# Performance work log

Hardware: AMD Instinct MI355X
Metric: run time of the kernel (lower is better)

The kernel has to match this reference:

```python
import jax, jax.numpy as jnp
import numpy as np

B, Tc, E, K, M, V = 8, 1024, 256, 8, 2048, 16
T1 = Tc * K          # penultimate layer length = 8192
TLAST = M * K        # last layer length = 16384


def setup_inputs() -> dict:
    key = jax.random.key(0)
    ks = jax.random.split(key, 12)
    x = jax.random.normal(ks[0], (B, Tc, E), jnp.float32)
    # penultimate values: exactly M 'mixed' tokens (value==2) per row, rest in {1,3}
    base = jnp.where(jnp.arange(T1) < M, 2, 1 + 2 * jax.random.randint(ks[1], (B, T1), 0, 2))
    perm = jnp.argsort(jax.random.uniform(ks[2], (B, T1)), axis=1)
    val1 = jnp.take_along_axis(base, perm, axis=1)
    vallast = 1 + 2 * jax.random.randint(ks[3], (B, TLAST), 0, 2)
    value = jnp.concatenate([val1, vallast], axis=1).astype(jnp.int64)
    depth = jnp.concatenate([jnp.full((B, T1), 5), jnp.full((B, TLAST), 6)], axis=1).astype(jnp.int64)
    pos = jax.random.randint(ks[4], (B, T1 + TLAST, 3), 0, 64).astype(jnp.int64)
    s = 0.02
    W1 = s * jax.random.normal(ks[5], (E, E, K), jnp.float32)  # ConvTranspose1d weight [in,out,k]
    b1 = s * jax.random.normal(ks[6], (E,), jnp.float32)
    W0 = s * jax.random.normal(ks[7], (E, E, K), jnp.float32)
    b0 = s * jax.random.normal(ks[8], (E,), jnp.float32)
    Wl = s * jax.random.normal(ks[9], (V + 1, E), jnp.float32)
    bl = s * jax.random.normal(ks[10], (V + 1,), jnp.float32)
    return {"x": x, "value": value, "depth": depth, "pos": pos, "num_mix": M,
            "W1": W1, "b1": b1, "W0": W0, "b0": b0, "Wl": Wl, "bl": bl}


def _deconv(x, W, b):
    # ConvTranspose1d with kernel=stride=K: each token expands to K tokens
    n, t, e = x.shape
    o = W.shape[1]
    y = jnp.einsum('nte,eoj->ntjo', x, W)  # [N,T,K,O]
    return y.reshape(n, t * W.shape[2], o) + b


def reference(x, value, depth, pos, num_mix, W1, b1, W0, b0, Wl, bl):
    n, tc, e = x.shape
    k = W1.shape[2]
    t1 = tc * k
    max_depth = jnp.max(depth)
    len_1 = jnp.sum(depth == max_depth - 1, axis=1)               # [N]
    tt = jnp.arange(t1)
    val_1 = jnp.where(tt[None, :] < len_1[:, None], value[:, :t1], 0)  # padded penultimate values
    mix_mask = val_1 == 2                                         # [N,T1]
    mix_1 = jnp.sum(mix_mask, axis=1)                             # [N]
    y_1 = _deconv(x, W1, b1)                                      # [N,T1,E]
    # stable pack: bring positions with value==2 to the front, keep order
    order = jnp.argsort(jnp.where(mix_mask, 0, 1), axis=1, stable=True)
    sel = order[:, :num_mix]                                      # [N,M]
    x_0 = jnp.take_along_axis(y_1, sel[:, :, None], axis=1)       # [N,M,E]
    valid = (jnp.arange(num_mix)[None, :] < mix_1[:, None]).astype(x_0.dtype)
    x_0 = x_0 * valid[:, :, None]                                 # zero-pad beyond per-row mix count
    y_0 = _deconv(x_0, W0, b0)                                    # [N,M*K,E]
    return y_0 @ Wl.T + bl                                        # [N,M*K,V+1]
```

## Files before the change

kernel.cpp:

```cpp
#include <hip/hip_runtime.h>

typedef __attribute__((ext_vector_type(8))) short bf16x8;
typedef __attribute__((ext_vector_type(4))) float f32x4;

#define BB 8
#define TC 1024
#define EE 256
#define KJ 8
#define MSEL 2048
#define V1 17
#define T1 8192
#define TTOT 24576
#define BI_TOT 16384
#define NCOLP 160
#define WSTRIDE 264

#define SCAL_OFF 0
#define GRP_OFF  1024
#define WFT_OFF  (GRP_OFF + 524288)
#define B2_OFF   (WFT_OFF + NCOLP*WSTRIDE*2)
#define BF0_OFF  (B2_OFF + 640)
#define WCT_OFF  (BF0_OFF + 128)

__device__ __forceinline__ unsigned short f2bf(float f) {
    union { float f; unsigned u; } x; x.f = f;
    unsigned r = x.u + 0x7fffu + ((x.u >> 16) & 1u);
    return (unsigned short)(r >> 16);
}
__device__ __forceinline__ float bf2f(unsigned short h) {
    union { unsigned u; float f; } x; x.u = ((unsigned)h) << 16;
    return x.f;
}

__global__ __launch_bounds__(256) void k_pre(const float* W0, const float* Wl, const int* depth,
                                             unsigned short* wfT, int* scal) {
    int bid = blockIdx.x, tid = threadIdx.x;
    __shared__ float w0s[EE * KJ];
    __shared__ float wls[V1 * 257];
    __shared__ int s_red[4];
    int em = bid;
    for (int idx = tid; idx < EE * KJ; idx += 256) w0s[idx] = W0[em * EE * KJ + idx];
    for (int idx = tid; idx < V1 * EE; idx += 256) {
        int v = idx >> 8, o = idx & 255;
        wls[v * 257 + o] = Wl[idx];
    }
    __syncthreads();
    if (tid < 136) {
        int j = tid / V1, v = tid - j * V1;
        float acc = 0.f;
        #pragma unroll 4
        for (int o = 0; o < EE; ++o) acc += w0s[o * KJ + j] * wls[v * 257 + o];
        wfT[(j * 20 + v) * WSTRIDE + em] = f2bf(acc);
    }
    if (bid < 8) {
        int b = bid;
        if (b == 0 && tid < 8) scal[33 + tid] = 0;
        const int4* dp = (const int4*)(depth + b * TTOT);
        int m = -2147483648;
        for (int i = tid; i < 6144; i += 256) {
            int4 d = dp[i];
            m = max(max(m, max(d.x, d.y)), max(d.z, d.w));
        }
        #pragma unroll
        for (int dd = 32; dd; dd >>= 1) m = max(m, __shfl_down(m, dd, 64));
        if ((tid & 63) == 0) s_red[tid >> 6] = m;
        __syncthreads();
        int bmax = max(max(s_red[0], s_red[1]), max(s_red[2], s_red[3]));
        if (tid == 0) scal[1 + b] = bmax;
        int c1 = 0, c2 = 0;
        for (int i = tid; i < 6144; i += 256) {
            int4 d = dp[i];
            c1 += (d.x == bmax) + (d.y == bmax) + (d.z == bmax) + (d.w == bmax);
            c2 += (d.x == bmax - 1) + (d.y == bmax - 1) + (d.z == bmax - 1) + (d.w == bmax - 1);
        }
        int cc = (c1 << 16) + c2;
        #pragma unroll
        for (int dd = 32; dd; dd >>= 1) cc += __shfl_down(cc, dd, 64);
        __syncthreads();
        if ((tid & 63) == 0) s_red[tid >> 6] = cc;
        __syncthreads();
        if (tid == 0) {
            int tot = s_red[0] + s_red[1] + s_red[2] + s_red[3];
            scal[9 + b] = tot >> 16;
            scal[17 + b] = tot & 0xffff;
        }
    }
}

__global__ __launch_bounds__(256) void k_mid(
        const int* value, const float* W1, const float* b1, const float* b0,
        const float* Wl, const float* bl,
        int* scal, int* groups, const unsigned short* wfT, float* bias2, float* bf0,
        unsigned short* wct) {
    int bid = blockIdx.x, tid = threadIdx.x;
    __shared__ __align__(16) unsigned short b1s[32 * WSTRIDE];
    __shared__ __align__(16) unsigned short af[NCOLP * WSTRIDE];
    __shared__ int s_wt[4], s_lcnt[8], s_lcnt2[8], s_lbase[8];
    if (bid < 64) {
        int g = bid >> 3;
        int e0 = (bid & 7) * 32;
        {
            int em_l = tid & 63;
            int eb = (tid >> 6) * 8;
            #pragma unroll
            for (int i = 0; i < 8; ++i) {
                int e = eb + i;
                #pragma unroll
                for (int c = 0; c < 4; ++c) {
                    int em = c * 64 + em_l;
                    b1s[e * WSTRIDE + em] = f2bf(W1[(e0 + e) * (EE * KJ) + em * KJ + g]);
                }
            }
        }
        for (int idx = tid; idx < 5120; idx += 256) {
            int row = idx >> 5, f = idx & 31;
            ((int4*)af)[row * 33 + f] = ((const int4*)wfT)[row * 33 + f];
        }
        __syncthreads();

        int w = tid >> 6, l = tid & 63;
        int ntile = w & 1, mhalf = w >> 1;
        int lr = l & 15, lq = l >> 4;
        f32x4 acc[5];
        #pragma unroll
        for (int t = 0; t < 5; ++t) acc[t] = (f32x4){0.f, 0.f, 0.f, 0.f};

        #pragma unroll
        for (int ch = 0; ch < 4; ++ch) {
            #pragma unroll
            for (int s = 0; s < 2; ++s) {
                bf16x8 bfr = *(const bf16x8*)&b1s[(ntile * 16 + lr) * WSTRIDE + ch * 64 + s * 32 + lq * 8];
                #pragma unroll
                for (int t = 0; t < 5; ++t) {
                    bf16x8 afr = *(const bf16x8*)&af[((mhalf * 5 + t) * 16 + lr) * WSTRIDE + ch * 64 + s * 32 + lq * 8];
                    acc[t] = __builtin_amdgcn_mfma_f32_16x16x32_bf16(afr, bfr, acc[t], 0, 0, 0);
                }
            }
        }
        #pragma unroll
        for (int t = 0; t < 5; ++t) {
            int m = (mhalf * 5 + t) * 16 + lq * 4;
            int n = e0 + ntile * 16 + lr;
            #pragma unroll
            for (int r = 0; r < 4; ++r)
                wct[(g * NCOLP + m + r) * WSTRIDE + n] = f2bf(acc[t][r]);
        }
        if (bid == 0) {
            for (int c = tid; c < NCOLP; c += 256) {
                int vv = c % 20;
                float s = 0.f;
                if (vv < V1) {
                    for (int e8 = 0; e8 < 32; ++e8) {
                        bf16x8 a8 = *(const bf16x8*)&af[c * WSTRIDE + e8 * 8];
                        #pragma unroll
                        for (int u = 0; u < 8; ++u)
                            s += b1[e8 * 8 + u] * bf2f((unsigned short)a8[u]);
                    }
                }
                bias2[c] = s;
            }
        } else if (bid == 1) {
            if (tid < V1) {
                float s = 0.f;
                #pragma unroll 4
                for (int e = 0; e < EE; ++e) s += b0[e] * Wl[tid * EE + e];
                bf0[tid] = s + bl[tid];
            }
        }
    } else {
        int b = bid - 64;
        int mb = scal[1 + b], cm = scal[9 + b], cm1 = scal[17 + b];
        int gmax = scal[1];
        #pragma unroll
        for (int q = 2; q <= 8; ++q) gmax = max(gmax, scal[q]);
        int len1 = (mb == gmax) ? cm1 : ((mb == gmax - 1) ? cm : 0);
        const int* vb = value + b * TTOT;
        int t0 = tid * 32;
        unsigned mask = 0;
        #pragma unroll
        for (int k = 0; k < 32; k += 4) {
            int4 v = *(const int4*)(vb + t0 + k);
            if (t0 + k + 0 < len1 && v.x == 2) mask |= 1u << (k + 0);
            if (t0 + k + 1 < len1 && v.y == 2) mask |= 1u << (k + 1);
            if (t0 + k + 2 < len1 && v.z == 2) mask |= 1u << (k + 2);
            if (t0 + k + 3 < len1 && v.w == 2) mask |= 1u << (k + 3);
        }
        int cnt = __popc(mask);
        int inc = cnt;
        #pragma unroll
        for (int d = 1; d < 64; d <<= 1) {
            int n = __shfl_up(inc, d, 64);
            if ((tid & 63) >= d) inc += n;
        }
        int lane = tid & 63, wid = tid >> 6;
        if (lane == 63) s_wt[wid] = inc;
        if (tid < 8) { s_lcnt[tid] = 0; s_lcnt2[tid] = 0; }
        __syncthreads();
        int woff = 0;
        for (int w = 0; w < wid; ++w) woff += s_wt[w];
        int off0 = woff + inc - cnt;
        int mix1 = s_wt[0] + s_wt[1] + s_wt[2] + s_wt[3];
        int mix1c = min(mix1, MSEL);
        {
            int off = off0;
            #pragma unroll
            for (int k = 0; k < 32; ++k) {
                if (mask & (1u << k)) {
                    if (off < MSEL) atomicAdd(&s_lcnt[(t0 + k) & 7], 1);
                    off++;
                }
            }
        }
        if (tid == 0 && mix1c < MSEL) atomicAdd(&s_lcnt[0], MSEL - mix1c);
        __syncthreads();
        if (tid < 8) s_lbase[tid] = atomicAdd(&scal[33 + tid], s_lcnt[tid]);
        __syncthreads();
        {
            int off = off0;
            #pragma unroll
            for (int k = 0; k < 32; ++k) {
                if (mask & (1u << k)) {
                    if (off < MSEL) {
                        int t = t0 + k;
                        int g = t & 7;
                        int ls = atomicAdd(&s_lcnt2[g], 1);
                        groups[g * BI_TOT + s_lbase[g] + ls] =
                            ((b * MSEL + off) << 11) | ((t >> 3) << 1) | 1;
                    }
                    off++;
                }
            }
        }
        for (int i = mix1c + tid; i < MSEL; i += 256) {
            int ls = atomicAdd(&s_lcnt2[0], 1);
            groups[s_lbase[0] + ls] = (b * MSEL + i) << 11;
        }
    }
}

__global__ __launch_bounds__(256) void k_main(const float* x, const unsigned short* wct,
        const int* scal, const int* groups, const float* bias2, const float* bf0, float* out) {
    int g = blockIdx.x >> 7;
    int tile0 = blockIdx.x & 127;
    int cntg = scal[33 + g];

    __shared__ __align__(16) unsigned short xs[32 * WSTRIDE];
    __shared__ __align__(16) unsigned short wts[NCOLP * 72];
    __shared__ int obase[32];
    __shared__ unsigned char vflag[32];
    int tid = threadIdx.x;
    const int4* wsrc = (const int4*)wct;
    int row8 = tid >> 3, q8 = tid & 7;
    int w = tid >> 6, l = tid & 63;
    int rw = w & 1, chalf = w >> 1;
    int lr = l & 15, lq = l >> 4;

    for (int tile = tile0; tile * 32 < cntg; tile += 128) {
        int nrows = min(32, cntg - tile * 32);
        int4 wreg[5];
        #pragma unroll
        for (int q = 0; q < 5; ++q)
            wreg[q] = wsrc[(g * NCOLP + row8 + q * 32) * 33 + q8];
        int pk = (row8 < nrows) ? groups[g * BI_TOT + tile * 32 + row8] : 0;
        int xo = ((pk >> 22) * TC + ((pk >> 1) & 1023)) * EE;
        float4 xr[8];
        #pragma unroll
        for (int i = 0; i < 8; ++i) xr[i] = *(const float4*)(x + xo + (q8 + 8 * i) * 4);

        __syncthreads();
        if (tid < 32) {
            int p2 = (tid < nrows) ? groups[g * BI_TOT + tile * 32 + tid] : 0;
            obase[tid] = (p2 >> 11) * 136;
            vflag[tid] = (tid < nrows) ? (unsigned char)(1 + (p2 & 1)) : (unsigned char)0;
        }
        #pragma unroll
        for (int i = 0; i < 8; ++i) {
            ushort4 pkv;
            pkv.x = f2bf(xr[i].x); pkv.y = f2bf(xr[i].y);
            pkv.z = f2bf(xr[i].z); pkv.w = f2bf(xr[i].w);
            *(ushort4*)&xs[row8 * WSTRIDE + (q8 + 8 * i) * 4] = pkv;
        }
        #pragma unroll
        for (int q = 0; q < 5; ++q)
            ((int4*)wts)[(row8 + q * 32) * 9 + q8] = wreg[q];
        #pragma unroll
        for (int q = 0; q < 5; ++q)
            wreg[q] = wsrc[(g * NCOLP + row8 + q * 32) * 33 + 8 + q8];
        __syncthreads();

        f32x4 acc[5];
        #pragma unroll
        for (int t = 0; t < 5; ++t) acc[t] = (f32x4){0.f, 0.f, 0.f, 0.f};

        for (int ch = 0; ch < 4; ++ch) {
            #pragma unroll
            for (int s = 0; s < 2; ++s) {
                bf16x8 afr = *(const bf16x8*)&xs[(rw * 16 + lr) * WSTRIDE + ch * 64 + s * 32 + lq * 8];
                #pragma unroll
                for (int t = 0; t < 5; ++t) {
                    bf16x8 bfr = *(const bf16x8*)&wts[((chalf * 5 + t) * 16 + lr) * 72 + s * 32 + lq * 8];
                    acc[t] = __builtin_amdgcn_mfma_f32_16x16x32_bf16(afr, bfr, acc[t], 0, 0, 0);
                }
            }
            if (ch < 3) {
                __syncthreads();
                #pragma unroll
                for (int q = 0; q < 5; ++q)
                    ((int4*)wts)[(row8 + q * 32) * 9 + q8] = wreg[q];
                if (ch < 2) {
                    #pragma unroll
                    for (int q = 0; q < 5; ++q)
                        wreg[q] = wsrc[(g * NCOLP + row8 + q * 32) * 33 + (ch + 2) * 8 + q8];
                }
                __syncthreads();
            }
        }
        #pragma unroll
        for (int t = 0; t < 5; ++t) {
            int col = (chalf * 5 + t) * 16 + lr;
            int j = col / 20, v = col % 20;
            if (v < V1) {
                float bb = bias2[col] + bf0[v];
                float b0v = bf0[v];
                #pragma unroll
                for (int r = 0; r < 4; ++r) {
                    int row = rw * 16 + lq * 4 + r;
                    int fl = vflag[row];
                    if (fl) out[obase[row] + j * V1 + v] = (fl == 2) ? (acc[t][r] + bb) : b0v;
                }
            }
        }
    }
}

extern "C" void kernel_launch(void* const* d_in, const int* in_sizes, int n_in,
                              void* d_out, int out_size, void* d_ws, size_t ws_size,
                              hipStream_t stream) {
    const float* x     = (const float*)d_in[0];
    const int*   value = (const int*)d_in[1];
    const int*   depth = (const int*)d_in[2];
    const float* W1    = (const float*)d_in[5];
    const float* b1    = (const float*)d_in[6];
    const float* W0    = (const float*)d_in[7];
    const float* b0    = (const float*)d_in[8];
    const float* Wl    = (const float*)d_in[9];
    const float* bl    = (const float*)d_in[10];
    float* out = (float*)d_out;
    char* ws = (char*)d_ws;

    int*            scal   = (int*)(ws + SCAL_OFF);
    int*            groups = (int*)(ws + GRP_OFF);
    unsigned short* wfT    = (unsigned short*)(ws + WFT_OFF);
    float*          bias2  = (float*)(ws + B2_OFF);
    float*          bf0    = (float*)(ws + BF0_OFF);
    unsigned short* wct    = (unsigned short*)(ws + WCT_OFF);

    k_pre <<<dim3(256),  dim3(256), 0, stream>>>(W0, Wl, depth, wfT, scal);
    k_mid <<<dim3(72),   dim3(256), 0, stream>>>(value, W1, b1, b0, Wl, bl,
                                                 scal, groups, wfT, bias2, bf0, wct);
    k_main<<<dim3(1024), dim3(256), 0, stream>>>(x, wct, scal, groups, bias2, bf0, out);
}
```

Before: 137.5 us.

## Pre-swizzle weights into MFMA fragment layout and read them directly from global

Stores the fused weight matrices (wfT and wct) in a packed layout that matches the MFMA operand fragment order, so each lane can load its bf16x8 operand straight from global memory. This removes the LDS staging, register double-buffering and per-chunk barriers in k_main and k_mid. It also moves the depth scan in k_pre to its own blocks and spreads the bias reductions (bias2, bf0) across extra k_mid blocks instead of doing them serially in one block. The cost is that weight reads now rely on L1/L2 hits rather than shared memory.

```diff
diff --git a/kernel.cpp b/kernel.cpp
--- a/kernel.cpp
+++ b/kernel.cpp
@@ -14,11 +14,16 @@
 #define BI_TOT 16384
 #define NCOLP 160
 #define WSTRIDE 264
+#define GSZ 40960
+
+__device__ __forceinline__ int pk_idx(int col, int e) {
+    return (((col >> 4) * 8 + (e >> 5)) << 9) + (((e >> 3) & 3) << 7) + ((col & 15) << 3) + (e & 7);
+}
 
 #define SCAL_OFF 0
 #define GRP_OFF  1024
 #define WFT_OFF  (GRP_OFF + 524288)
-#define B2_OFF   (WFT_OFF + NCOLP*WSTRIDE*2)
+#define B2_OFF   (WFT_OFF + GSZ*2)
 #define BF0_OFF  (B2_OFF + 640)
 #define WCT_OFF  (BF0_OFF + 128)
 
@@ -30,6 +35,18 @@
 __device__ __forceinline__ float bf2f(unsigned short h) {
     union { unsigned u; float f; } x; x.u = ((unsigned)h) << 16;
     return x.f;
+}
+
+__device__ __forceinline__ float blockReduceSum256(float v) {
+    __shared__ float sm[4];
+    #pragma unroll
+    for (int d = 32; d; d >>= 1) v += __shfl_down(v, d, 64);
+    int lane = threadIdx.x & 63, wid = threadIdx.x >> 6;
+    if (lane == 0) sm[wid] = v;
+    __syncthreads();
+    float r = sm[0] + sm[1] + sm[2] + sm[3];
+    __syncthreads();
+    return r;
 }
 
 __global__ __launch_bounds__(256) void k_pre(const float* W0, const float* Wl, const int* depth,
@@ -38,22 +55,23 @@
     __shared__ float w0s[EE * KJ];
     __shared__ float wls[V1 * 257];
     __shared__ int s_red[4];
-    int em = bid;
-    for (int idx = tid; idx < EE * KJ; idx += 256) w0s[idx] = W0[em * EE * KJ + idx];
-    for (int idx = tid; idx < V1 * EE; idx += 256) {
-        int v = idx >> 8, o = idx & 255;
-        wls[v * 257 + o] = Wl[idx];
-    }
-    __syncthreads();
-    if (tid < 136) {
-        int j = tid / V1, v = tid - j * V1;
-        float acc = 0.f;
-        #pragma unroll 4
-        for (int o = 0; o < EE; ++o) acc += w0s[o * KJ + j] * wls[v * 257 + o];
-        wfT[(j * 20 + v) * WSTRIDE + em] = f2bf(acc);
-    }
-    if (bid < 8) {
-        int b = bid;
+    if (bid < 256) {
+        int em = bid;
+        for (int idx = tid; idx < EE * KJ; idx += 256) w0s[idx] = W0[em * EE * KJ + idx];
+        for (int idx = tid; idx < V1 * EE; idx += 256) {
+            int v = idx >> 8, o = idx & 255;
+            wls[v * 257 + o] = Wl[idx];
+        }
+        __syncthreads();
+        if (tid < 136) {
+            int j = tid / V1, v = tid - j * V1;
+            float acc = 0.f;
+            #pragma unroll 4
+            for (int o = 0; o < EE; ++o) acc += w0s[o * KJ + j] * wls[v * 257 + o];
+            wfT[pk_idx(j * 20 + v, em)] = f2bf(acc);
+        }
+    } else {
+        int b = bid - 256;
         if (b == 0 && tid < 8) scal[33 + tid] = 0;
         const int4* dp = (const int4*)(depth + b * TTOT);
         int m = -2147483648;
@@ -94,7 +112,6 @@
         unsigned short* wct) {
     int bid = blockIdx.x, tid = threadIdx.x;
     __shared__ __align__(16) unsigned short b1s[32 * WSTRIDE];
-    __shared__ __align__(16) unsigned short af[NCOLP * WSTRIDE];
     __shared__ int s_wt[4], s_lcnt[8], s_lcnt2[8], s_lbase[8];
     if (bid < 64) {
         int g = bid >> 3;
@@ -112,10 +129,6 @@
                 }
             }
         }
-        for (int idx = tid; idx < 5120; idx += 256) {
-            int row = idx >> 5, f = idx & 31;
-            ((int4*)af)[row * 33 + f] = ((const int4*)wfT)[row * 33 + f];
-        }
         __syncthreads();
 
         int w = tid >> 6, l = tid & 63;
@@ -132,42 +145,22 @@
                 bf16x8 bfr = *(const bf16x8*)&b1s[(ntile * 16 + lr) * WSTRIDE + ch * 64 + s * 32 + lq * 8];
                 #pragma unroll
                 for (int t = 0; t < 5; ++t) {
-                    bf16x8 afr = *(const bf16x8*)&af[((mhalf * 5 + t) * 16 + lr) * WSTRIDE + ch * 64 + s * 32 + lq * 8];
+                    bf16x8 afr = *(const bf16x8*)&wfT[(((mhalf * 5 + t) * 8 + ch * 2 + s) << 9) + l * 8];
                     acc[t] = __builtin_amdgcn_mfma_f32_16x16x32_bf16(afr, bfr, acc[t], 0, 0, 0);
                 }
             }
         }
         #pragma unroll
         for (int t = 0; t < 5; ++t) {
-            int m = (mhalf * 5 + t) * 16 + lq * 4;
-            int n = e0 + ntile * 16 + lr;
-            #pragma unroll
-            for (int r = 0; r < 4; ++r)
-                wct[(g * NCOLP + m + r) * WSTRIDE + n] = f2bf(acc[t][r]);
-        }
-        if (bid == 0) {
-            for (int c = tid; c < NCOLP; c += 256) {
-                int vv = c % 20;
-                float s = 0.f;
-                if (vv < V1) {
-                    for (int e8 = 0; e8 < 32; ++e8) {
-                        bf16x8 a8 = *(const bf16x8*)&af[c * WSTRIDE + e8 * 8];
-                        #pragma unroll
-                        for (int u = 0; u < 8; ++u)
-                            s += b1[e8 * 8 + u] * bf2f((unsigned short)a8[u]);
-                    }
-                }
-                bias2[c] = s;
-            }
-        } else if (bid == 1) {
-            if (tid < V1) {
-                float s = 0.f;
-                #pragma unroll 4
-                for (int e = 0; e < EE; ++e) s += b0[e] * Wl[tid * EE + e];
-                bf0[tid] = s + bl[tid];
-            }
-        }
-    } else {
+            int ct = mhalf * 5 + t;
+            int e = e0 + ntile * 16 + lr;
+            #pragma unroll
+            for (int r = 0; r < 4; ++r) {
+                int col = ct * 16 + lq * 4 + r;
+                wct[g * GSZ + pk_idx(col, e)] = f2bf(acc[t][r]);
+            }
+        }
+    } else if (bid < 72) {
         int b = bid - 64;
         int mb = scal[1 + b], cm = scal[9 + b], cm1 = scal[17 + b];
         int gmax = scal[1];
@@ -235,6 +228,19 @@
             int ls = atomicAdd(&s_lcnt2[0], 1);
             groups[s_lbase[0] + ls] = (b * MSEL + i) << 11;
         }
+    } else if (bid < 89) {
+        int v = bid - 72;
+        float s = blockReduceSum256(b0[tid] * Wl[v * EE + tid]);
+        if (tid == 0) bf0[v] = s + bl[v];
+    } else {
+        #pragma unroll
+        for (int r = 0; r < 2; ++r) {
+            int c17 = (bid - 89) * 2 + r;
+            int j = c17 / V1, v = c17 - j * V1;
+            int colP = j * 20 + v;
+            float s = blockReduceSum256(b1[tid] * bf2f(wfT[pk_idx(colP, tid)]));
+            if (tid == 0) bias2[colP] = s;
+        }
     }
 }
 
@@ -245,34 +251,30 @@
     int cntg = scal[33 + g];
 
     __shared__ __align__(16) unsigned short xs[32 * WSTRIDE];
-    __shared__ __align__(16) unsigned short wts[NCOLP * 72];
     __shared__ int obase[32];
     __shared__ unsigned char vflag[32];
     int tid = threadIdx.x;
-    const int4* wsrc = (const int4*)wct;
     int row8 = tid >> 3, q8 = tid & 7;
     int w = tid >> 6, l = tid & 63;
     int rw = w & 1, chalf = w >> 1;
     int lr = l & 15, lq = l >> 4;
+    const unsigned short* wg = wct + g * GSZ;
 
     for (int tile = tile0; tile * 32 < cntg; tile += 128) {
         int nrows = min(32, cntg - tile * 32);
-        int4 wreg[5];
-        #pragma unroll
-        for (int q = 0; q < 5; ++q)
-            wreg[q] = wsrc[(g * NCOLP + row8 + q * 32) * 33 + q8];
+        __syncthreads();
         int pk = (row8 < nrows) ? groups[g * BI_TOT + tile * 32 + row8] : 0;
-        int xo = ((pk >> 22) * TC + ((pk >> 1) & 1023)) * EE;
-        float4 xr[8];
-        #pragma unroll
-        for (int i = 0; i < 8; ++i) xr[i] = *(const float4*)(x + xo + (q8 + 8 * i) * 4);
-
-        __syncthreads();
         if (tid < 32) {
             int p2 = (tid < nrows) ? groups[g * BI_TOT + tile * 32 + tid] : 0;
             obase[tid] = (p2 >> 11) * 136;
             vflag[tid] = (tid < nrows) ? (unsigned char)(1 + (p2 & 1)) : (unsigned char)0;
         }
+        int bi = pk >> 11;
+        int xo = ((bi >> 11) * TC + ((pk >> 1) & 1023)) * EE;
+        const float* xp = x + xo;
+        float4 xr[8];
+        #pragma unroll
+        for (int i = 0; i < 8; ++i) xr[i] = *(const float4*)(xp + (q8 + 8 * i) * 4);
         #pragma unroll
         for (int i = 0; i < 8; ++i) {
             ushort4 pkv;
@@ -280,39 +282,21 @@
             pkv.z = f2bf(xr[i].z); pkv.w = f2bf(xr[i].w);
             *(ushort4*)&xs[row8 * WSTRIDE + (q8 + 8 * i) * 4] = pkv;
         }
-        #pragma unroll
-        for (int q = 0; q < 5; ++q)
-            ((int4*)wts)[(row8 + q * 32) * 9 + q8] = wreg[q];
-        #pragma unroll
-        for (int q = 0; q < 5; ++q)
-            wreg[q] = wsrc[(g * NCOLP + row8 + q * 32) * 33 + 8 + q8];
         __syncthreads();
 
         f32x4 acc[5];
         #pragma unroll
         for (int t = 0; t < 5; ++t) acc[t] = (f32x4){0.f, 0.f, 0.f, 0.f};
-
+        #pragma unroll
         for (int ch = 0; ch < 4; ++ch) {
             #pragma unroll
             for (int s = 0; s < 2; ++s) {
                 bf16x8 afr = *(const bf16x8*)&xs[(rw * 16 + lr) * WSTRIDE + ch * 64 + s * 32 + lq * 8];
                 #pragma unroll
                 for (int t = 0; t < 5; ++t) {
-                    bf16x8 bfr = *(const bf16x8*)&wts[((chalf * 5 + t) * 16 + lr) * 72 + s * 32 + lq * 8];
+                    bf16x8 bfr = *(const bf16x8*)&wg[(((chalf * 5 + t) * 8 + ch * 2 + s) << 9) + l * 8];
                     acc[t] = __builtin_amdgcn_mfma_f32_16x16x32_bf16(afr, bfr, acc[t], 0, 0, 0);
                 }
-            }
-            if (ch < 3) {
-                __syncthreads();
-                #pragma unroll
-                for (int q = 0; q < 5; ++q)
-                    ((int4*)wts)[(row8 + q * 32) * 9 + q8] = wreg[q];
-                if (ch < 2) {
-                    #pragma unroll
-                    for (int q = 0; q < 5; ++q)
-                        wreg[q] = wsrc[(g * NCOLP + row8 + q * 32) * 33 + (ch + 2) * 8 + q8];
-                }
-                __syncthreads();
             }
         }
         #pragma unroll
@@ -355,8 +339,8 @@
     float*          bf0    = (float*)(ws + BF0_OFF);
     unsigned short* wct    = (unsigned short*)(ws + WCT_OFF);
 
-    k_pre <<<dim3(256),  dim3(256), 0, stream>>>(W0, Wl, depth, wfT, scal);
-    k_mid <<<dim3(72),   dim3(256), 0, stream>>>(value, W1, b1, b0, Wl, bl,
+    k_pre <<<dim3(264),  dim3(256), 0, stream>>>(W0, Wl, depth, wfT, scal);
+    k_mid <<<dim3(157),  dim3(256), 0, stream>>>(value, W1, b1, b0, Wl, bl,
                                                  scal, groups, wfT, bias2, bf0, wct);
     k_main<<<dim3(1024), dim3(256), 0, stream>>>(x, wct, scal, groups, bias2, bf0, out);
 }
```

Measured after the change: 116.5 us. 1.18x faster.
